# Performance work log

Hardware: AMD Instinct MI355X
Metric: run time of the kernel (lower is better)

The kernel has to match this reference:

```python
import jax, jax.numpy as jnp
import numpy as np

D, NH, DH, DM = 1024, 16, 64, 4096
B, S = 2, 2048
EPS = 1e-5


def _layernorm(x, w, b):
    mu = jnp.mean(x, axis=-1, keepdims=True)
    var = jnp.mean((x - mu) ** 2, axis=-1, keepdims=True)
    return (x - mu) * jax.lax.rsqrt(var + EPS) * w + b


def setup_inputs() -> dict:
    key = jax.random.key(0)
    ks = jax.random.split(key, 8)
    scale = D ** (-0.5)
    x = jax.random.normal(ks[0], (B, S, D), dtype=jnp.float32)
    WQ = jax.random.normal(ks[1], (NH, D, DH), dtype=jnp.float32) * scale
    WK = jax.random.normal(ks[2], (NH, D, DH), dtype=jnp.float32) * scale
    WV = jax.random.normal(ks[3], (NH, D, DH), dtype=jnp.float32) * scale
    WO = jax.random.normal(ks[4], (NH, DH, D), dtype=jnp.float32) * scale
    # MLP: torch Linear default init ~ U(-1/sqrt(fan_in), 1/sqrt(fan_in)); stored as [in, out]
    W1 = jax.random.uniform(ks[5], (D, DM), dtype=jnp.float32, minval=-1.0, maxval=1.0) * D ** (-0.5)
    b1 = jnp.zeros((DM,), dtype=jnp.float32)
    W2 = jax.random.uniform(ks[6], (DM, D), dtype=jnp.float32, minval=-1.0, maxval=1.0) * DM ** (-0.5)
    b2 = jnp.zeros((D,), dtype=jnp.float32)
    ln1_w = jnp.ones((D,), dtype=jnp.float32)
    ln1_b = jnp.zeros((D,), dtype=jnp.float32)
    ln2_w = jnp.ones((D,), dtype=jnp.float32)
    ln2_b = jnp.zeros((D,), dtype=jnp.float32)
    return {"x": x, "WQ": WQ, "WK": WK, "WV": WV, "WO": WO,
            "W1": W1, "b1": b1, "W2": W2, "b2": b2,
            "ln1_w": ln1_w, "ln1_b": ln1_b, "ln2_w": ln2_w, "ln2_b": ln2_b}


def reference(x, WQ, WK, WV, WO, W1, b1, W2, b2, ln1_w, ln1_b, ln2_w, ln2_b):
    s = x.shape[1]
    dh = WQ.shape[-1]
    r = x
    h = _layernorm(x, ln1_w, ln1_b)
    # batched across all heads (original loops over h; math identical)
    Q = jnp.einsum('bsd,hde->bhse', h, WQ)
    K = jnp.einsum('bsd,hde->bhse', h, WK)
    V = jnp.einsum('bsd,hde->bhse', h, WV)
    scores = jnp.einsum('bhqe,bhke->bhqk', Q, K) / jnp.sqrt(jnp.float32(dh))
    causal = jnp.tril(jnp.ones((s, s), dtype=bool))  # True = keep
    scores = jnp.where(causal, scores, -jnp.inf)
    attn = jax.nn.softmax(scores, axis=-1)
    ctx = jnp.einsum('bhqk,bhke->bhqe', attn, V)
    ao = jnp.einsum('bhqe,hed->bqd', ctx, WO)  # sum over heads
    x = r + ao
    h2 = _layernorm(x, ln2_w, ln2_b)
    mlp = jax.nn.gelu(h2 @ W1 + b1, approximate=False) @ W2 + b2
    return x + mlp
```

## Files before the change

kernel.cpp:

```cpp
#include <hip/hip_runtime.h>
#include <hip/hip_bf16.h>
#include <cstdint>

#define D_MODEL 1024
#define NHEADS 16
#define DHEAD 64
#define DMLP 4096
#define BATCH 2
#define SEQ 2048
#define ROWS (BATCH*SEQ)
#define LN_EPS 1e-5f

typedef __attribute__((ext_vector_type(8))) short short8;
typedef __attribute__((ext_vector_type(4))) float f32x4;

typedef const __attribute__((address_space(1))) uint32_t* gas_ptr;
typedef __attribute__((address_space(3))) uint32_t* las_ptr;

__device__ __forceinline__ short f2bf(float f) {
  union { float f; uint32_t u; } v; v.f = f;
  uint32_t r = v.u + 0x7FFFu + ((v.u >> 16) & 1u);
  return (short)(r >> 16);
}
__device__ __forceinline__ float bf2f(short s) {
  union { uint32_t u; float f; } v; v.u = ((uint32_t)(uint16_t)s) << 16;
  return v.f;
}

__global__ void ln_kernel(const float* __restrict__ x, const float* __restrict__ w,
                          const float* __restrict__ b, short* __restrict__ out) {
  int row = blockIdx.x;
  int t = threadIdx.x;
  const float4 v = ((const float4*)(x + (size_t)row * D_MODEL))[t];
  float s = v.x + v.y + v.z + v.w;
  float s2 = v.x*v.x + v.y*v.y + v.z*v.z + v.w*v.w;
#pragma unroll
  for (int k = 1; k < 64; k <<= 1) { s += __shfl_xor(s, k); s2 += __shfl_xor(s2, k); }
  __shared__ float red[8];
  int wv = t >> 6;
  if ((t & 63) == 0) { red[wv] = s; red[wv + 4] = s2; }
  __syncthreads();
  s = red[0] + red[1] + red[2] + red[3];
  s2 = red[4] + red[5] + red[6] + red[7];
  float mu = s * (1.0f / D_MODEL);
  float var = s2 * (1.0f / D_MODEL) - mu * mu;
  float rstd = rsqrtf(var + LN_EPS);
  const float4 wv4 = ((const float4*)w)[t];
  const float4 bv4 = ((const float4*)b)[t];
  short4 o4;
  o4.x = f2bf((v.x - mu) * rstd * wv4.x + bv4.x);
  o4.y = f2bf((v.y - mu) * rstd * wv4.y + bv4.y);
  o4.z = f2bf((v.z - mu) * rstd * wv4.z + bv4.z);
  o4.w = f2bf((v.w - mu) * rstd * wv4.w + bv4.w);
  *(short4*)(out + (size_t)row * D_MODEL + t * 4) = o4;
}

__global__ __launch_bounds__(256) void transpose_tile(const float* __restrict__ src, short* __restrict__ dst,
                                                      int R, int C, int srcMatStride) {
  __shared__ float tile[64][65];
  const int m = blockIdx.z;
  const int r0 = blockIdx.y * 64, c0 = blockIdx.x * 64;
  const int tx = threadIdx.x & 15, ty = threadIdx.x >> 4;
  const float* s = src + (size_t)m * srcMatStride + (size_t)r0 * C + c0;
#pragma unroll
  for (int i = 0; i < 4; i++) {
    float4 v = *(const float4*)(s + (size_t)(ty + i * 16) * C + tx * 4);
    tile[ty + i * 16][tx * 4 + 0] = v.x;
    tile[ty + i * 16][tx * 4 + 1] = v.y;
    tile[ty + i * 16][tx * 4 + 2] = v.z;
    tile[ty + i * 16][tx * 4 + 3] = v.w;
  }
  __syncthreads();
  short* d = dst + (size_t)m * C * R + (size_t)c0 * R + r0;
#pragma unroll
  for (int p = 0; p < 4; p++) {
    int c = ty + p * 16;
    int r4 = tx * 4;
    short4 o;
    o.x = f2bf(tile[r4 + 0][c]);
    o.y = f2bf(tile[r4 + 1][c]);
    o.z = f2bf(tile[r4 + 2][c]);
    o.w = f2bf(tile[r4 + 3][c]);
    *(short4*)(d + (size_t)c * R + r4) = o;
  }
}

template<int EPI>
__global__ __launch_bounds__(256) void gemm_bt(const short* __restrict__ A, const short* __restrict__ BT,
                        const float* __restrict__ bias, const float* __restrict__ resid,
                        float* __restrict__ outf, short* __restrict__ outb,
                        int M, int N, int K) {
  __shared__ alignas(16) short As[2][128 * 32];
  __shared__ alignas(16) short Bs[2][128 * 32];
  const int t = threadIdx.x;
  const int l = t & 63;
  const int w = t >> 6;
  const int row0 = blockIdx.y * 128, col0 = blockIdx.x * 128;

  f32x4 acc[4][4] = {};

  const int srow = w * 16 + (l >> 2);
  const int cs8 = ((l & 3) ^ (srow & 3)) * 8;
  const short* Abase = A + (size_t)(row0 + srow) * K + cs8;
  const short* Bbase = BT + (size_t)(col0 + srow) * K + cs8;
  char* AsB = (char*)As;
  char* BsB = (char*)Bs;
  const int ldsoff = w * 1024 + l * 16;

  const int wr = (w >> 1) * 64, wc = (w & 1) * 64;
  const int l15 = l & 15, l4 = l >> 4;
  const int rchunk = (l4 ^ (l15 & 3)) * 8;

  __builtin_amdgcn_global_load_lds((gas_ptr)(Abase),          (las_ptr)(AsB + ldsoff),        16, 0, 0);
  __builtin_amdgcn_global_load_lds((gas_ptr)(Abase + 64 * K), (las_ptr)(AsB + 4096 + ldsoff), 16, 0, 0);
  __builtin_amdgcn_global_load_lds((gas_ptr)(Bbase),          (las_ptr)(BsB + ldsoff),        16, 0, 0);
  __builtin_amdgcn_global_load_lds((gas_ptr)(Bbase + 64 * K), (las_ptr)(BsB + 4096 + ldsoff), 16, 0, 0);
  __syncthreads();

  const int nk = K >> 5;
  for (int ti = 0; ti < nk; ti++) {
    const int cur = ti & 1;
    if (ti + 1 < nk) {
      const int nb = (cur ^ 1) * 8192;
      const int k0 = (ti + 1) << 5;
      __builtin_amdgcn_global_load_lds((gas_ptr)(Abase + k0),          (las_ptr)(AsB + nb + ldsoff),        16, 0, 0);
      __builtin_amdgcn_global_load_lds((gas_ptr)(Abase + 64 * K + k0), (las_ptr)(AsB + nb + 4096 + ldsoff), 16, 0, 0);
      __builtin_amdgcn_global_load_lds((gas_ptr)(Bbase + k0),          (las_ptr)(BsB + nb + ldsoff),        16, 0, 0);
      __builtin_amdgcn_global_load_lds((gas_ptr)(Bbase + 64 * K + k0), (las_ptr)(BsB + nb + 4096 + ldsoff), 16, 0, 0);
    }
    const short* Ab = &As[cur][0];
    const short* Bb = &Bs[cur][0];
    short8 a[4], bfr[4];
#pragma unroll
    for (int m = 0; m < 4; m++) a[m]   = *(const short8*)&Ab[(wr + m * 16 + l15) * 32 + rchunk];
#pragma unroll
    for (int n = 0; n < 4; n++) bfr[n] = *(const short8*)&Bb[(wc + n * 16 + l15) * 32 + rchunk];
#pragma unroll
    for (int m = 0; m < 4; m++)
#pragma unroll
      for (int n = 0; n < 4; n++)
        acc[m][n] = __builtin_amdgcn_mfma_f32_16x16x32_bf16(a[m], bfr[n], acc[m][n], 0, 0, 0);
    __syncthreads();
  }

#pragma unroll
  for (int m = 0; m < 4; m++) {
#pragma unroll
    for (int n = 0; n < 4; n++) {
#pragma unroll
      for (int j = 0; j < 4; j++) {
        int R_ = row0 + wr + m * 16 + l4 * 4 + j;
        int C_ = col0 + wc + n * 16 + l15;
        float v = acc[m][n][j];
        size_t o = (size_t)R_ * N + C_;
        if (EPI == 0) {
          outb[o] = f2bf(v);
        } else if (EPI == 1) {
          outf[o] = v + resid[o];
        } else if (EPI == 2) {
          float xx = v + bias[C_];
          outb[o] = f2bf(0.5f * xx * (1.0f + erff(xx * 0.70710678118f)));
        } else {
          outf[o] = v + bias[C_] + resid[o];
        }
      }
    }
  }
}

__device__ __forceinline__ void attn_step(
    int kt_, int qt, int bufP,
    const short* __restrict__ base, const short* __restrict__ vbase,
    short8& vWA, short8& vWB,
    short8& vLA, short8& vLB,
    const short8 qf[2],
    char* KsB, char* VtB, char* PlB,
    f32x4 acc[4], float mrun[4], float lrun[4],
    int w, int l, int q0, int vr, int vd0)
{
  const int l15 = l & 15, l4 = l >> 4;
  const int bufQ = bufP ^ 1;
  if (kt_ < qt) {
#pragma unroll
    for (int i = 0; i < 8; i++) {
      int d = vd0 + i;
      int cs = (vr >> 2) ^ ((d >> 3) & 7);
      uint32_t val = (uint32_t)(uint16_t)vWA[i] | ((uint32_t)(uint16_t)vWB[i] << 16);
      *(uint32_t*)(VtB + bufQ * 9216 + d * 144 + cs * 16 + (vr & 3) * 4) = val;
    }
#pragma unroll
    for (int i = 0; i < 2; i++) {
      int g = (w * 2 + i) * 64 + l;
      int key = g >> 3, ck = g & 7;
      const short* src = base + (size_t)((kt_ + 1) * 64 + key) * 3072 + 1024 + ((ck ^ (key & 7)) * 8);
      __builtin_amdgcn_global_load_lds((gas_ptr)src, (las_ptr)(KsB + bufQ * 8192 + g * 16), 16, 0, 0);
    }
  }
  if (kt_ + 2 <= qt) {
    vLA = *(const short8*)(vbase + (size_t)((kt_ + 2) * 64 + 2 * vr) * 3072);
    vLB = *(const short8*)(vbase + (size_t)((kt_ + 2) * 64 + 2 * vr + 1) * 3072);
  }

  f32x4 sc[4];
#pragma unroll
  for (int cb = 0; cb < 4; cb++) {
    f32x4 s = {};
    int key = cb * 16 + l15;
#pragma unroll
    for (int c = 0; c < 2; c++) {
      int ck = (c * 4 + l4) ^ (key & 7);
      short8 kf = *(const short8*)(KsB + bufP * 8192 + key * 128 + ck * 16);
      s = __builtin_amdgcn_mfma_f32_16x16x32_bf16(qf[c], kf, s, 0, 0, 0);
    }
    sc[cb] = s;
  }

  const bool lastt = (kt_ == qt);
  float alpha[4];
#pragma unroll
  for (int jj = 0; jj < 4; jj++) {
    int qg = q0 + l4 * 4 + jj;
    float s0 = sc[0][jj] * 0.125f;
    float s1 = sc[1][jj] * 0.125f;
    float s2 = sc[2][jj] * 0.125f;
    float s3 = sc[3][jj] * 0.125f;
    if (lastt) {
      int kg = kt_ * 64 + l15;
      if (kg      > qg) s0 = -1e30f;
      if (kg + 16 > qg) s1 = -1e30f;
      if (kg + 32 > qg) s2 = -1e30f;
      if (kg + 48 > qg) s3 = -1e30f;
    }
    float rm = fmaxf(fmaxf(s0, s1), fmaxf(s2, s3));
    rm = fmaxf(rm, __shfl_xor(rm, 1));
    rm = fmaxf(rm, __shfl_xor(rm, 2));
    rm = fmaxf(rm, __shfl_xor(rm, 4));
    rm = fmaxf(rm, __shfl_xor(rm, 8));
    float nm = fmaxf(mrun[jj], rm);
    float al = __expf(mrun[jj] - nm);
    mrun[jj] = nm;
    float p0 = __expf(s0 - nm), p1 = __expf(s1 - nm);
    float p2 = __expf(s2 - nm), p3 = __expf(s3 - nm);
    float ps = p0 + p1 + p2 + p3;
    ps += __shfl_xor(ps, 1);
    ps += __shfl_xor(ps, 2);
    ps += __shfl_xor(ps, 4);
    ps += __shfl_xor(ps, 8);
    lrun[jj] = lrun[jj] * al + ps;
    alpha[jj] = al;
    short* pr = (short*)(PlB + (l4 * 4 + jj) * 144);
    pr[l15]      = f2bf(p0);
    pr[16 + l15] = f2bf(p1);
    pr[32 + l15] = f2bf(p2);
    pr[48 + l15] = f2bf(p3);
  }
#pragma unroll
  for (int db = 0; db < 4; db++) {
    f32x4 a = acc[db];
    a[0] *= alpha[0]; a[1] *= alpha[1]; a[2] *= alpha[2]; a[3] *= alpha[3];
    acc[db] = a;
  }
#pragma unroll
  for (int kc = 0; kc < 2; kc++) {
    short8 pf = *(const short8*)(PlB + l15 * 144 + kc * 64 + l4 * 16);
#pragma unroll
    for (int db = 0; db < 4; db++) {
      int d = db * 16 + l15;
      int cs = (kc * 4 + l4) ^ ((d >> 3) & 7);
      short8 vf = *(const short8*)(VtB + bufP * 9216 + d * 144 + cs * 16);
      acc[db] = __builtin_amdgcn_mfma_f32_16x16x32_bf16(pf, vf, acc[db], 0, 0, 0);
    }
  }
}

__global__ __launch_bounds__(256) void attn_mfma(const short* __restrict__ qkv, short* __restrict__ ctx) {
  __shared__ alignas(16) short Ks[2 * 64 * 64];
  __shared__ alignas(16) short Vt[2 * 64 * 72];
  __shared__ alignas(16) short Pl[4][16 * 72];
  const int t = threadIdx.x;
  const int l = t & 63;
  const int w = t >> 6;
  const int l15 = l & 15, l4 = l >> 4;
  const int bh = blockIdx.x;
  const int b = bh >> 4, h = bh & 15;
  const int qt = (gridDim.y - 1) - blockIdx.y;
  const int q0 = qt * 64 + w * 16;

  const short* base = qkv + (size_t)b * SEQ * 3072 + h * 64;

  short8 qf[2];
#pragma unroll
  for (int c = 0; c < 2; c++)
    qf[c] = *(const short8*)(base + (size_t)(q0 + l15) * 3072 + c * 32 + l4 * 8);

  const int vr = t >> 3;
  const int vd0 = (t & 7) * 8;
  const short* vbase = base + 2048 + vd0;

  char* KsB = (char*)Ks;
  char* VtB = (char*)Vt;
  char* PlB = (char*)&Pl[w][0];

  short8 va0, vb0, va1, vb1;
  va0 = *(const short8*)(vbase + (size_t)(2 * vr) * 3072);
  vb0 = *(const short8*)(vbase + (size_t)(2 * vr + 1) * 3072);
  if (qt >= 1) {
    va1 = *(const short8*)(vbase + (size_t)(64 + 2 * vr) * 3072);
    vb1 = *(const short8*)(vbase + (size_t)(64 + 2 * vr + 1) * 3072);
  }
#pragma unroll
  for (int i = 0; i < 8; i++) {
    int d = vd0 + i;
    int cs = (vr >> 2) ^ ((d >> 3) & 7);
    uint32_t val = (uint32_t)(uint16_t)va0[i] | ((uint32_t)(uint16_t)vb0[i] << 16);
    *(uint32_t*)(VtB + d * 144 + cs * 16 + (vr & 3) * 4) = val;
  }
#pragma unroll
  for (int i = 0; i < 2; i++) {
    int g = (w * 2 + i) * 64 + l;
    int key = g >> 3, ck = g & 7;
    const short* src = base + (size_t)key * 3072 + 1024 + ((ck ^ (key & 7)) * 8);
    __builtin_amdgcn_global_load_lds((gas_ptr)src, (las_ptr)(KsB + g * 16), 16, 0, 0);
  }
  __syncthreads();

  f32x4 acc[4] = {};
  float mrun[4] = {-1e30f, -1e30f, -1e30f, -1e30f};
  float lrun[4] = {0.f, 0.f, 0.f, 0.f};

  int kt = 0;
  while (true) {
    attn_step(kt, qt, 0, base, vbase, va1, vb1, va0, vb0, qf,
              KsB, VtB, PlB, acc, mrun, lrun, w, l, q0, vr, vd0);
    __syncthreads();
    if (++kt > qt) break;
    attn_step(kt, qt, 1, base, vbase, va0, vb0, va1, vb1, qf,
              KsB, VtB, PlB, acc, mrun, lrun, w, l, q0, vr, vd0);
    __syncthreads();
    if (++kt > qt) break;
  }

  float inv[4];
#pragma unroll
  for (int jj = 0; jj < 4; jj++) inv[jj] = 1.0f / lrun[jj];
  short* obase = ctx + (size_t)(b * SEQ + q0) * D_MODEL + h * 64;
#pragma unroll
  for (int db = 0; db < 4; db++)
#pragma unroll
    for (int jj = 0; jj < 4; jj++)
      obase[(size_t)(l4 * 4 + jj) * D_MODEL + db * 16 + l15] = f2bf(acc[db][jj] * inv[jj]);
}

extern "C" void kernel_launch(void* const* d_in, const int* in_sizes, int n_in,
                              void* d_out, int out_size, void* d_ws, size_t ws_size,
                              hipStream_t stream) {
  (void)in_sizes; (void)n_in; (void)out_size; (void)ws_size;
  const float* x    = (const float*)d_in[0];
  const float* WQ   = (const float*)d_in[1];
  const float* WK   = (const float*)d_in[2];
  const float* WV   = (const float*)d_in[3];
  const float* WO   = (const float*)d_in[4];
  const float* W1   = (const float*)d_in[5];
  const float* b1   = (const float*)d_in[6];
  const float* W2   = (const float*)d_in[7];
  const float* b2   = (const float*)d_in[8];
  const float* ln1w = (const float*)d_in[9];
  const float* ln1b = (const float*)d_in[10];
  const float* ln2w = (const float*)d_in[11];
  const float* ln2b = (const float*)d_in[12];
  float* out = (float*)d_out;

  char* p = (char*)d_ws;
  short* h1    = (short*)p; p += (size_t)ROWS * D_MODEL * 2;
  short* ctx   = (short*)p; p += (size_t)ROWS * D_MODEL * 2;
  short* h2    = (short*)p; p += (size_t)ROWS * D_MODEL * 2;
  short* m1    = (short*)p; p += (size_t)ROWS * DMLP * 2;
  short* wqkvT = (short*)p; p += (size_t)3 * D_MODEL * D_MODEL * 2;
  short* woT   = (short*)p; p += (size_t)D_MODEL * D_MODEL * 2;
  short* w1T   = (short*)p; p += (size_t)D_MODEL * DMLP * 2;
  short* w2T   = (short*)p; p += (size_t)D_MODEL * DMLP * 2;
  short* qkv   = (short*)p; p += (size_t)ROWS * 3 * D_MODEL * 2;

  transpose_tile<<<dim3(1, 16, 16), 256, 0, stream>>>(WQ, wqkvT,                  1024, 64, D_MODEL * DHEAD);
  transpose_tile<<<dim3(1, 16, 16), 256, 0, stream>>>(WK, wqkvT + 1024 * 1024,    1024, 64, D_MODEL * DHEAD);
  transpose_tile<<<dim3(1, 16, 16), 256, 0, stream>>>(WV, wqkvT + 2 * 1024 * 1024, 1024, 64, D_MODEL * DHEAD);
  transpose_tile<<<dim3(16, 16, 1), 256, 0, stream>>>(WO, woT, 1024, 1024, 0);
  transpose_tile<<<dim3(64, 16, 1), 256, 0, stream>>>(W1, w1T, 1024, 4096, 0);
  transpose_tile<<<dim3(16, 64, 1), 256, 0, stream>>>(W2, w2T, 4096, 1024, 0);

  ln_kernel<<<ROWS, 256, 0, stream>>>(x, ln1w, ln1b, h1);
  gemm_bt<0><<<dim3(3 * D_MODEL / 128, ROWS / 128), 256, 0, stream>>>(
      h1, wqkvT, nullptr, nullptr, nullptr, qkv, ROWS, 3 * D_MODEL, D_MODEL);
  attn_mfma<<<dim3(BATCH * NHEADS, SEQ / 64), 256, 0, stream>>>(qkv, ctx);
  gemm_bt<1><<<dim3(D_MODEL / 128, ROWS / 128), 256, 0, stream>>>(
      ctx, woT, nullptr, x, out, nullptr, ROWS, D_MODEL, D_MODEL);
  ln_kernel<<<ROWS, 256, 0, stream>>>(out, ln2w, ln2b, h2);
  gemm_bt<2><<<dim3(DMLP / 128, ROWS / 128), 256, 0, stream>>>(
      h2, w1T, b1, nullptr, nullptr, m1, ROWS, DMLP, D_MODEL);
  gemm_bt<3><<<dim3(D_MODEL / 128, ROWS / 128), 256, 0, stream>>>(
      m1, w2T, b2, out, out, nullptr, ROWS, D_MODEL, DMLP);
}
```

Before: 308.1 us.

## Add 256x256 LDS-DMA GEMM with XCD swizzle and split-K for MLP down-proj

Introduces a 512-thread GEMM with 256x256 tiles, direct global-to-LDS loads with an XOR swizzle, double-buffered 128KB LDS, and XCD-aware block remapping. It replaces the QKV and MLP GEMMs. The down-projection uses a 4-way split-K whose partials go to reused workspace buffers and are summed by a separate reduce kernel. The aim is more data reuse per tile and better CU occupancy for the small-N GEMM, at the cost of extra fp32 partial traffic, an extra launch, and low occupancy from the large LDS footprint.

```diff
diff --git a/kernel.cpp b/kernel.cpp
--- a/kernel.cpp
+++ b/kernel.cpp
@@ -82,6 +82,135 @@
     o.z = f2bf(tile[r4 + 2][c]);
     o.w = f2bf(tile[r4 + 3][c]);
     *(short4*)(d + (size_t)c * R + r4) = o;
+  }
+}
+
+template<int EPI>
+__global__ __launch_bounds__(512) void gemm256(const short* __restrict__ A, const short* __restrict__ BT,
+    const float* __restrict__ bias, const float* __restrict__ resid,
+    float* __restrict__ outf, short* __restrict__ outb,
+    float* __restrict__ pp1, float* __restrict__ pp2, float* __restrict__ pp3,
+    int M, int N, int K, int LDA, int LDB) {
+  extern __shared__ __align__(16) char ldsB[];
+  const int t = threadIdx.x;
+  const int l = t & 63, w = t >> 6;
+  const int l15 = l & 15, l4 = l >> 4;
+  const int gx = gridDim.x, gy = gridDim.y;
+  const int nwg = gx * gy;
+  int orig = blockIdx.x + gx * blockIdx.y;
+  { int q = nwg >> 3, r = nwg & 7, xcd = orig & 7, lin = orig >> 3;
+    orig = (xcd < r ? xcd * (q + 1) : r * (q + 1) + (xcd - r) * q) + lin; }
+  const int bx = orig % gx, by = orig / gx;
+  const int z = blockIdx.z;
+  const size_t kz = (size_t)z * K;
+  const int row0 = by * 256, col0 = bx * 256;
+  const int wrr = (w >> 2) * 128;
+  const int wc = (w & 3) * 64;
+
+  f32x4 acc[8][4] = {};
+
+  auto stage = [&](int p, int kt1, int c1) {
+    const int s = p >> 1;
+    const bool isB = p & 1;
+    const short* mat = isB ? BT : A;
+    const int ld = isB ? LDB : LDA;
+    const int b0 = isB ? col0 : row0;
+    const size_t koff = kz + (size_t)kt1 * 64 + s * 32;
+    char* dbase = ldsB + (isB ? 65536 : 0) + (c1 * 2 + s) * 16384;
+#pragma unroll
+    for (int j = 0; j < 2; j++) {
+      int G = (w * 2 + j) * 64 + l;
+      int gr = G >> 2, ch = G & 3;
+      const short* src = mat + (size_t)(b0 + gr) * ld + koff + ((ch ^ (gr & 3)) * 8);
+      __builtin_amdgcn_global_load_lds((gas_ptr)src, (las_ptr)(dbase + G * 16), 16, 0, 0);
+    }
+  };
+
+  stage(0, 0, 0); stage(1, 0, 0); stage(2, 0, 0); stage(3, 0, 0);
+  asm volatile("s_waitcnt vmcnt(4)" ::: "memory");
+  __builtin_amdgcn_s_barrier();
+
+  const int nk = K >> 6;
+  short8 bf[4];
+  for (int kt = 0; kt < nk; kt++) {
+    const int c = kt & 1;
+    const bool pf = (kt + 1 < nk);
+#pragma unroll 4
+    for (int p = 0; p < 4; p++) {
+      const int s = p >> 1;
+      const int fr0 = (p & 1) * 4;
+      const char* abase = ldsB + (c * 2 + s) * 16384;
+      const char* bbase = ldsB + 65536 + (c * 2 + s) * 16384;
+      short8 af[4];
+#pragma unroll
+      for (int i = 0; i < 4; i++) {
+        int R = wrr + (fr0 + i) * 16 + l15;
+        af[i] = *(const short8*)(abase + R * 64 + ((l4 ^ (R & 3)) * 16));
+      }
+      if ((p & 1) == 0) {
+#pragma unroll
+        for (int i = 0; i < 4; i++) {
+          int Cc = wc + i * 16 + l15;
+          bf[i] = *(const short8*)(bbase + Cc * 64 + ((l4 ^ (Cc & 3)) * 16));
+        }
+      }
+      if (pf) stage(p, kt + 1, c ^ 1);
+      __builtin_amdgcn_s_barrier();
+      __builtin_amdgcn_s_setprio(1);
+#pragma unroll
+      for (int i = 0; i < 4; i++)
+#pragma unroll
+        for (int n = 0; n < 4; n++)
+          acc[fr0 + i][n] = __builtin_amdgcn_mfma_f32_16x16x32_bf16(af[i], bf[n], acc[fr0 + i][n], 0, 0, 0);
+      __builtin_amdgcn_s_setprio(0);
+      if (p == 1) {
+        if (pf) { asm volatile("s_waitcnt vmcnt(4)" ::: "memory"); }
+        else    { asm volatile("s_waitcnt vmcnt(0)" ::: "memory"); }
+      } else if (p == 3) {
+        if (pf) { asm volatile("s_waitcnt vmcnt(4)" ::: "memory"); }
+      }
+      __builtin_amdgcn_s_barrier();
+    }
+  }
+
+#pragma unroll
+  for (int fr = 0; fr < 8; fr++) {
+#pragma unroll
+    for (int fc = 0; fc < 4; fc++) {
+#pragma unroll
+      for (int j = 0; j < 4; j++) {
+        int R = row0 + wrr + fr * 16 + l4 * 4 + j;
+        int C = col0 + wc + fc * 16 + l15;
+        float v = acc[fr][fc][j];
+        size_t o = (size_t)R * N + C;
+        if (EPI == 0) {
+          outb[o] = f2bf(v);
+        } else if (EPI == 2) {
+          float xx = v + bias[C];
+          outb[o] = f2bf(0.5f * xx * (1.0f + erff(xx * 0.70710678118f)));
+        } else if (EPI == 3) {
+          if (z == 0) outf[o] = v + bias[C] + resid[o];
+          else if (z == 1) pp1[o] = v;
+          else if (z == 2) pp2[o] = v;
+          else pp3[o] = v;
+        }
+      }
+    }
+  }
+}
+
+__global__ void reduce3(float* __restrict__ out, const float* __restrict__ a,
+                        const float* __restrict__ b, const float* __restrict__ c, int n4) {
+  for (int i = blockIdx.x * 256 + threadIdx.x; i < n4; i += gridDim.x * 256) {
+    float4 o = ((float4*)out)[i];
+    float4 x = ((const float4*)a)[i];
+    float4 y = ((const float4*)b)[i];
+    float4 zz = ((const float4*)c)[i];
+    o.x += x.x + y.x + zz.x;
+    o.y += x.y + y.y + zz.y;
+    o.z += x.z + y.z + zz.z;
+    o.w += x.w + y.w + zz.w;
+    ((float4*)out)[i] = o;
   }
 }
 
@@ -381,22 +510,34 @@
   short* w2T   = (short*)p; p += (size_t)D_MODEL * DMLP * 2;
   short* qkv   = (short*)p; p += (size_t)ROWS * 3 * D_MODEL * 2;
 
-  transpose_tile<<<dim3(1, 16, 16), 256, 0, stream>>>(WQ, wqkvT,                  1024, 64, D_MODEL * DHEAD);
-  transpose_tile<<<dim3(1, 16, 16), 256, 0, stream>>>(WK, wqkvT + 1024 * 1024,    1024, 64, D_MODEL * DHEAD);
+  float* fp1 = (float*)h1;
+  float* fp2 = (float*)qkv;
+  float* fp3 = (float*)wqkvT;
+
+  hipFuncSetAttribute((const void*)gemm256<0>, hipFuncAttributeMaxDynamicSharedMemorySize, 131072);
+  hipFuncSetAttribute((const void*)gemm256<2>, hipFuncAttributeMaxDynamicSharedMemorySize, 131072);
+  hipFuncSetAttribute((const void*)gemm256<3>, hipFuncAttributeMaxDynamicSharedMemorySize, 131072);
+
+  transpose_tile<<<dim3(1, 16, 16), 256, 0, stream>>>(WQ, wqkvT,                   1024, 64, D_MODEL * DHEAD);
+  transpose_tile<<<dim3(1, 16, 16), 256, 0, stream>>>(WK, wqkvT + 1024 * 1024,     1024, 64, D_MODEL * DHEAD);
   transpose_tile<<<dim3(1, 16, 16), 256, 0, stream>>>(WV, wqkvT + 2 * 1024 * 1024, 1024, 64, D_MODEL * DHEAD);
   transpose_tile<<<dim3(16, 16, 1), 256, 0, stream>>>(WO, woT, 1024, 1024, 0);
   transpose_tile<<<dim3(64, 16, 1), 256, 0, stream>>>(W1, w1T, 1024, 4096, 0);
   transpose_tile<<<dim3(16, 64, 1), 256, 0, stream>>>(W2, w2T, 4096, 1024, 0);
 
   ln_kernel<<<ROWS, 256, 0, stream>>>(x, ln1w, ln1b, h1);
-  gemm_bt<0><<<dim3(3 * D_MODEL / 128, ROWS / 128), 256, 0, stream>>>(
-      h1, wqkvT, nullptr, nullptr, nullptr, qkv, ROWS, 3 * D_MODEL, D_MODEL);
+  gemm256<0><<<dim3(3 * D_MODEL / 256, ROWS / 256, 1), 512, 131072, stream>>>(
+      h1, wqkvT, nullptr, nullptr, nullptr, qkv, nullptr, nullptr, nullptr,
+      ROWS, 3 * D_MODEL, D_MODEL, D_MODEL, D_MODEL);
   attn_mfma<<<dim3(BATCH * NHEADS, SEQ / 64), 256, 0, stream>>>(qkv, ctx);
   gemm_bt<1><<<dim3(D_MODEL / 128, ROWS / 128), 256, 0, stream>>>(
       ctx, woT, nullptr, x, out, nullptr, ROWS, D_MODEL, D_MODEL);
   ln_kernel<<<ROWS, 256, 0, stream>>>(out, ln2w, ln2b, h2);
-  gemm_bt<2><<<dim3(DMLP / 128, ROWS / 128), 256, 0, stream>>>(
-      h2, w1T, b1, nullptr, nullptr, m1, ROWS, DMLP, D_MODEL);
-  gemm_bt<3><<<dim3(D_MODEL / 128, ROWS / 128), 256, 0, stream>>>(
-      m1, w2T, b2, out, out, nullptr, ROWS, D_MODEL, DMLP);
-}
+  gemm256<2><<<dim3(DMLP / 256, ROWS / 256, 1), 512, 131072, stream>>>(
+      h2, w1T, b1, nullptr, nullptr, m1, nullptr, nullptr, nullptr,
+      ROWS, DMLP, D_MODEL, D_MODEL, D_MODEL);
+  gemm256<3><<<dim3(D_MODEL / 256, ROWS / 256, 4), 512, 131072, stream>>>(
+      m1, w2T, b2, out, out, nullptr, fp1, fp2, fp3,
+      ROWS, D_MODEL, D_MODEL, DMLP, DMLP);
+  reduce3<<<2048, 256, 0, stream>>>(out, fp1, fp2, fp3, ROWS * D_MODEL / 4);
+}
```

Result: slower. 365.3 us (+18.6%).

## Triple-buffer GEMM LDS pipeline and split-K the N=1024 projection GEMMs

Applied to the files above, without the earlier changes.

The GEMM now uses three LDS stages, prefetching two k-tiles ahead. It replaces __syncthreads with explicit vmcnt waits plus s_barrier, and changes the LDS swizzle pattern. The output-projection and MLP-down GEMMs, which launch only 256 blocks, are split along K into two halves via blockIdx.z, with the second half written to a float scratch buffer and added back by a reduce kernel. This raises occupancy and memory-latency hiding, at the cost of extra LDS, an extra partial-sum round trip through memory and two extra launches.

```diff
diff --git a/kernel.cpp b/kernel.cpp
--- a/kernel.cpp
+++ b/kernel.cpp
@@ -87,60 +87,67 @@
 
 template<int EPI>
 __global__ __launch_bounds__(256) void gemm_bt(const short* __restrict__ A, const short* __restrict__ BT,
-                        const float* __restrict__ bias, const float* __restrict__ resid,
-                        float* __restrict__ outf, short* __restrict__ outb,
-                        int M, int N, int K) {
-  __shared__ alignas(16) short As[2][128 * 32];
-  __shared__ alignas(16) short Bs[2][128 * 32];
+    const float* __restrict__ bias, const float* __restrict__ resid,
+    float* __restrict__ outf, short* __restrict__ outb, float* __restrict__ part,
+    int M, int N, int K, int LDA, int LDB) {
+  __shared__ alignas(16) short As[3][4096];
+  __shared__ alignas(16) short Bs[3][4096];
   const int t = threadIdx.x;
-  const int l = t & 63;
-  const int w = t >> 6;
+  const int l = t & 63, w = t >> 6;
+  const int l15 = l & 15, l4 = l >> 4;
   const int row0 = blockIdx.y * 128, col0 = blockIdx.x * 128;
-
+  if (EPI == 5) {
+    A  += (size_t)blockIdx.z * K;
+    BT += (size_t)blockIdx.z * K;
+  }
   f32x4 acc[4][4] = {};
 
-  const int srow = w * 16 + (l >> 2);
-  const int cs8 = ((l & 3) ^ (srow & 3)) * 8;
-  const short* Abase = A + (size_t)(row0 + srow) * K + cs8;
-  const short* Bbase = BT + (size_t)(col0 + srow) * K + cs8;
+  const int gr = w * 16 + (l >> 2);
+  const int c8 = ((l & 3) ^ ((l >> 3) & 3)) * 8;
+  const short* Ab0 = A  + (size_t)(row0 + gr) * LDA + c8;
+  const short* Ab1 = A  + (size_t)(row0 + 64 + gr) * LDA + c8;
+  const short* Bb0 = BT + (size_t)(col0 + gr) * LDB + c8;
+  const short* Bb1 = BT + (size_t)(col0 + 64 + gr) * LDB + c8;
   char* AsB = (char*)As;
   char* BsB = (char*)Bs;
-  const int ldsoff = w * 1024 + l * 16;
+  const int soff = w * 1024 + l * 16;
+
+  auto stg = [&](int ti) {
+    const int bo = (ti % 3) * 8192;
+    const int k0 = ti << 5;
+    __builtin_amdgcn_global_load_lds((gas_ptr)(Ab0 + k0), (las_ptr)(AsB + bo + soff),        16, 0, 0);
+    __builtin_amdgcn_global_load_lds((gas_ptr)(Ab1 + k0), (las_ptr)(AsB + bo + 4096 + soff), 16, 0, 0);
+    __builtin_amdgcn_global_load_lds((gas_ptr)(Bb0 + k0), (las_ptr)(BsB + bo + soff),        16, 0, 0);
+    __builtin_amdgcn_global_load_lds((gas_ptr)(Bb1 + k0), (las_ptr)(BsB + bo + 4096 + soff), 16, 0, 0);
+  };
+
+  const int nk = K >> 5;
+  stg(0);
+  if (nk > 1) stg(1);
+  asm volatile("s_waitcnt vmcnt(4)" ::: "memory");
+  __builtin_amdgcn_s_barrier();
 
   const int wr = (w >> 1) * 64, wc = (w & 1) * 64;
-  const int l15 = l & 15, l4 = l >> 4;
-  const int rchunk = (l4 ^ (l15 & 3)) * 8;
-
-  __builtin_amdgcn_global_load_lds((gas_ptr)(Abase),          (las_ptr)(AsB + ldsoff),        16, 0, 0);
-  __builtin_amdgcn_global_load_lds((gas_ptr)(Abase + 64 * K), (las_ptr)(AsB + 4096 + ldsoff), 16, 0, 0);
-  __builtin_amdgcn_global_load_lds((gas_ptr)(Bbase),          (las_ptr)(BsB + ldsoff),        16, 0, 0);
-  __builtin_amdgcn_global_load_lds((gas_ptr)(Bbase + 64 * K), (las_ptr)(BsB + 4096 + ldsoff), 16, 0, 0);
-  __syncthreads();
-
-  const int nk = K >> 5;
+  const int rch = (l4 ^ ((l15 >> 1) & 3)) * 16;
+  const char* Arow = AsB + (wr >> 6) * 4096 + l15 * 64 + rch;
+  const char* Brow = BsB + (wc >> 6) * 4096 + l15 * 64 + rch;
+
   for (int ti = 0; ti < nk; ti++) {
-    const int cur = ti & 1;
-    if (ti + 1 < nk) {
-      const int nb = (cur ^ 1) * 8192;
-      const int k0 = (ti + 1) << 5;
-      __builtin_amdgcn_global_load_lds((gas_ptr)(Abase + k0),          (las_ptr)(AsB + nb + ldsoff),        16, 0, 0);
-      __builtin_amdgcn_global_load_lds((gas_ptr)(Abase + 64 * K + k0), (las_ptr)(AsB + nb + 4096 + ldsoff), 16, 0, 0);
-      __builtin_amdgcn_global_load_lds((gas_ptr)(Bbase + k0),          (las_ptr)(BsB + nb + ldsoff),        16, 0, 0);
-      __builtin_amdgcn_global_load_lds((gas_ptr)(Bbase + 64 * K + k0), (las_ptr)(BsB + nb + 4096 + ldsoff), 16, 0, 0);
-    }
-    const short* Ab = &As[cur][0];
-    const short* Bb = &Bs[cur][0];
+    const int bo = (ti % 3) * 8192;
+    if (ti + 2 < nk) stg(ti + 2);
     short8 a[4], bfr[4];
 #pragma unroll
-    for (int m = 0; m < 4; m++) a[m]   = *(const short8*)&Ab[(wr + m * 16 + l15) * 32 + rchunk];
-#pragma unroll
-    for (int n = 0; n < 4; n++) bfr[n] = *(const short8*)&Bb[(wc + n * 16 + l15) * 32 + rchunk];
+    for (int m = 0; m < 4; m++) a[m]   = *(const short8*)(Arow + bo + m * 1024);
+#pragma unroll
+    for (int n = 0; n < 4; n++) bfr[n] = *(const short8*)(Brow + bo + n * 1024);
 #pragma unroll
     for (int m = 0; m < 4; m++)
 #pragma unroll
       for (int n = 0; n < 4; n++)
         acc[m][n] = __builtin_amdgcn_mfma_f32_16x16x32_bf16(a[m], bfr[n], acc[m][n], 0, 0, 0);
-    __syncthreads();
+    if (ti + 2 < nk)      { asm volatile("s_waitcnt vmcnt(4)" ::: "memory"); }
+    else if (ti + 1 < nk) { asm volatile("s_waitcnt vmcnt(0)" ::: "memory"); }
+    __builtin_amdgcn_s_barrier();
   }
 
 #pragma unroll
@@ -155,16 +162,24 @@
         size_t o = (size_t)R_ * N + C_;
         if (EPI == 0) {
           outb[o] = f2bf(v);
-        } else if (EPI == 1) {
-          outf[o] = v + resid[o];
         } else if (EPI == 2) {
           float xx = v + bias[C_];
           outb[o] = f2bf(0.5f * xx * (1.0f + erff(xx * 0.70710678118f)));
-        } else {
-          outf[o] = v + bias[C_] + resid[o];
+        } else if (EPI == 5) {
+          if (blockIdx.z == 0) outf[o] = v + (bias ? bias[C_] : 0.0f) + resid[o];
+          else part[o] = v;
         }
       }
     }
+  }
+}
+
+__global__ void reduce1(float* __restrict__ out, const float* __restrict__ p, int n4) {
+  for (int i = blockIdx.x * 256 + threadIdx.x; i < n4; i += gridDim.x * 256) {
+    float4 o = ((float4*)out)[i];
+    float4 q = ((const float4*)p)[i];
+    o.x += q.x; o.y += q.y; o.z += q.z; o.w += q.w;
+    ((float4*)out)[i] = o;
   }
 }
 
@@ -381,8 +396,10 @@
   short* w2T   = (short*)p; p += (size_t)D_MODEL * DMLP * 2;
   short* qkv   = (short*)p; p += (size_t)ROWS * 3 * D_MODEL * 2;
 
-  transpose_tile<<<dim3(1, 16, 16), 256, 0, stream>>>(WQ, wqkvT,                  1024, 64, D_MODEL * DHEAD);
-  transpose_tile<<<dim3(1, 16, 16), 256, 0, stream>>>(WK, wqkvT + 1024 * 1024,    1024, 64, D_MODEL * DHEAD);
+  float* fp1 = (float*)qkv;
+
+  transpose_tile<<<dim3(1, 16, 16), 256, 0, stream>>>(WQ, wqkvT,                   1024, 64, D_MODEL * DHEAD);
+  transpose_tile<<<dim3(1, 16, 16), 256, 0, stream>>>(WK, wqkvT + 1024 * 1024,     1024, 64, D_MODEL * DHEAD);
   transpose_tile<<<dim3(1, 16, 16), 256, 0, stream>>>(WV, wqkvT + 2 * 1024 * 1024, 1024, 64, D_MODEL * DHEAD);
   transpose_tile<<<dim3(16, 16, 1), 256, 0, stream>>>(WO, woT, 1024, 1024, 0);
   transpose_tile<<<dim3(64, 16, 1), 256, 0, stream>>>(W1, w1T, 1024, 4096, 0);
@@ -390,13 +407,19 @@
 
   ln_kernel<<<ROWS, 256, 0, stream>>>(x, ln1w, ln1b, h1);
   gemm_bt<0><<<dim3(3 * D_MODEL / 128, ROWS / 128), 256, 0, stream>>>(
-      h1, wqkvT, nullptr, nullptr, nullptr, qkv, ROWS, 3 * D_MODEL, D_MODEL);
+      h1, wqkvT, nullptr, nullptr, nullptr, qkv, nullptr,
+      ROWS, 3 * D_MODEL, D_MODEL, D_MODEL, D_MODEL);
   attn_mfma<<<dim3(BATCH * NHEADS, SEQ / 64), 256, 0, stream>>>(qkv, ctx);
-  gemm_bt<1><<<dim3(D_MODEL / 128, ROWS / 128), 256, 0, stream>>>(
-      ctx, woT, nullptr, x, out, nullptr, ROWS, D_MODEL, D_MODEL);
+  gemm_bt<5><<<dim3(D_MODEL / 128, ROWS / 128, 2), 256, 0, stream>>>(
+      ctx, woT, nullptr, x, out, nullptr, fp1,
+      ROWS, D_MODEL, D_MODEL / 2, D_MODEL, D_MODEL);
+  reduce1<<<2048, 256, 0, stream>>>(out, fp1, ROWS * D_MODEL / 4);
   ln_kernel<<<ROWS, 256, 0, stream>>>(out, ln2w, ln2b, h2);
   gemm_bt<2><<<dim3(DMLP / 128, ROWS / 128), 256, 0, stream>>>(
-      h2, w1T, b1, nullptr, nullptr, m1, ROWS, DMLP, D_MODEL);
-  gemm_bt<3><<<dim3(D_MODEL / 128, ROWS / 128), 256, 0, stream>>>(
-      m1, w2T, b2, out, out, nullptr, ROWS, D_MODEL, DMLP);
-}
+      h2, w1T, b1, nullptr, nullptr, m1, nullptr,
+      ROWS, DMLP, D_MODEL, D_MODEL, D_MODEL);
+  gemm_bt<5><<<dim3(D_MODEL / 128, ROWS / 128, 2), 256, 0, stream>>>(
+      m1, w2T, b2, out, out, nullptr, fp1,
+      ROWS, D_MODEL, DMLP / 2, DMLP, DMLP);
+  reduce1<<<2048, 256, 0, stream>>>(out, fp1, ROWS * D_MODEL / 4);
+}
```

Result: slower. 315.9 us (+2.5%).
